# Optimization experiments

Measured on AMD Instinct MI355X. Metric: run time of the kernel, lower is better.

The kernel has to match this reference:

```python
import jax, jax.numpy as jnp
import numpy as np

B, S, E, H, W, G = 1, 2048, 1024, 16, 512, 16
HD = E // H

def setup_inputs() -> dict:
    key = jax.random.key(0)
    ks = jax.random.split(key, 12)
    s = 1.0 / np.sqrt(E)
    inp = {
        'query': jax.random.normal(ks[0], (B, S, E), jnp.float32),
        'key':   jax.random.normal(ks[1], (B, S, E), jnp.float32),
        'value': jax.random.normal(ks[2], (B, S, E), jnp.float32),
        'is_global': jnp.broadcast_to(jnp.arange(S) < G, (B, S)),
        'Wq': jax.random.uniform(ks[3], (E, E), jnp.float32, -s, s),
        'bq': jax.random.uniform(ks[4], (E,),   jnp.float32, -s, s),
        'Wk': jax.random.uniform(ks[5], (E, E), jnp.float32, -s, s),
        'bk': jax.random.uniform(ks[6], (E,),   jnp.float32, -s, s),
        'Wv': jax.random.uniform(ks[7], (E, E), jnp.float32, -s, s),
        'bv': jax.random.uniform(ks[8], (E,),   jnp.float32, -s, s),
        'Wo': jax.random.uniform(ks[9], (E, E), jnp.float32, -s, s),
        'bo': jax.random.uniform(ks[10], (E,),  jnp.float32, -s, s),
    }
    return inp

def reference(query, key, value, is_global, Wq, bq, Wk, bk, Wv, bv, Wo, bo):
    # Linear projections (torch Linear: x @ W.T + b), reshape to [B,H,S,HD]
    def proj(x, Wt, b):
        return (x @ Wt.T + b).reshape(B, S, H, HD).transpose(0, 2, 1, 3)
    q = proj(query, Wq, bq)
    k = proj(key,   Wk, bk)
    v = proj(value, Wv, bv)

    scores = jnp.einsum('bhqd,bhkd->bhqk', q, k) / np.sqrt(HD)  # [B,H,S,S]

    idx = jnp.arange(S)
    window_mask = jnp.abs(idx[None, :] - idx[:, None]) <= W      # [S,S]
    combined = (window_mask[None, None]
                | is_global[:, None, None, :]    # global keys
                | is_global[:, None, :, None])   # global queries
    scores = jnp.where(combined, scores, -jnp.inf)

    attn = jax.nn.softmax(scores, axis=-1)  # dropout is identity in eval
    out = jnp.einsum('bhqk,bhkd->bhqd', attn, v)
    out = out.transpose(0, 2, 1, 3).reshape(B, S, E)
    return out @ Wo.T + bo
```

## Files before the change

kernel.cpp:

```cpp
#include <hip/hip_runtime.h>
#include <hip/hip_bf16.h>
#include <stdint.h>

#define S_LEN 2048
#define E_DIM 1024
#define N_HEAD 16
#define HD 64
#define WIN 512

typedef __attribute__((ext_vector_type(4))) float f32x4;
typedef __attribute__((ext_vector_type(8))) short bf16x8;
typedef __attribute__((ext_vector_type(8))) unsigned short u16x8;

__device__ __forceinline__ unsigned f2bf2(float lo, float hi) {
  __hip_bfloat162 h = __float22bfloat162_rn(make_float2(lo, hi));
  return *reinterpret_cast<unsigned*>(&h);
}
__device__ __forceinline__ unsigned short f2bf(float f) {
  __hip_bfloat16 h = __float2bfloat16(f);
  return *reinterpret_cast<unsigned short*>(&h);
}
__device__ __forceinline__ float bf2f(unsigned short u) {
  union { unsigned u; float f; } v; v.u = (unsigned)u << 16; return v.f;
}

__device__ __forceinline__ void gl2lds16(const void* g, void* l) {
  __builtin_amdgcn_global_load_lds((const __attribute__((address_space(1))) void*)g,
                                   (__attribute__((address_space(3))) void*)l, 16, 0, 0);
}

__global__ __launch_bounds__(256) void convert_kernel(
    const float* __restrict__ q, const float* __restrict__ k, const float* __restrict__ v,
    const float* __restrict__ wq, const float* __restrict__ wk,
    const float* __restrict__ wv, const float* __restrict__ wo,
    unsigned short* __restrict__ dst, const int* __restrict__ gm,
    unsigned char* __restrict__ kmask, unsigned char* __restrict__ bflag) {
  const size_t SE = (size_t)S_LEN * E_DIM, EE = (size_t)E_DIM * E_DIM;
  if (blockIdx.x == 0) {
    __shared__ int badw;
    int tid = threadIdx.x;
    if (tid == 0) badw = 0;
    __syncthreads();
    for (int i = tid; i < S_LEN / 4; i += 256) {
      int vv = gm[i];
      if (vv != 0 && vv != 1) atomicOr(&badw, 1);
    }
    __syncthreads();
    const int bytes = badw;
    const unsigned char* gb = (const unsigned char*)gm;
    for (int i = tid; i < S_LEN; i += 256)
      kmask[i] = bytes ? (unsigned char)(gb[i] != 0) : (unsigned char)(gm[i] != 0);
    if (tid < S_LEN / 64) {
      unsigned char any = 0;
      for (int j = 0; j < 64; ++j) {
        int i = tid * 64 + j;
        any |= bytes ? (unsigned char)(gb[i] != 0) : (unsigned char)(gm[i] != 0);
      }
      bflag[tid] = any;
    }
  }
  size_t i = ((size_t)blockIdx.x * 256 + threadIdx.x) * 8;
  const float* src;
  size_t off;
  if (i < SE) { src = q; off = i; }
  else if (i < 2 * SE) { src = k; off = i - SE; }
  else if (i < 3 * SE) { src = v; off = i - 2 * SE; }
  else if (i < 3 * SE + EE) { src = wq; off = i - 3 * SE; }
  else if (i < 3 * SE + 2 * EE) { src = wk; off = i - 3 * SE - EE; }
  else if (i < 3 * SE + 3 * EE) { src = wv; off = i - 3 * SE - 2 * EE; }
  else { src = wo; off = i - 3 * SE - 3 * EE; }
  f32x4 x0 = *(const f32x4*)(src + off);
  f32x4 x1 = *(const f32x4*)(src + off + 4);
  union { u16x8 v; unsigned u[4]; } o;
  o.u[0] = f2bf2(x0[0], x0[1]); o.u[1] = f2bf2(x0[2], x0[3]);
  o.u[2] = f2bf2(x1[0], x1[1]); o.u[3] = f2bf2(x1[2], x1[3]);
  *(u16x8*)(dst + i) = o.v;
}

template <int BN, int OUTMODE>
__device__ __forceinline__ void gemm_body(const unsigned short* __restrict__ A,
                                          const unsigned short* __restrict__ B,
                                          const float* __restrict__ bias,
                                          void* __restrict__ Out_) {
  __shared__ unsigned short As[64][64];
  __shared__ unsigned short Bs[BN][64];
  constexpr int MI = (BN == 128) ? 2 : 1;
  const int tid = threadIdx.x;
  const int wid = tid >> 6, lane = tid & 63;
  const int a = lane & 15, g = lane >> 4;
  const int m0 = blockIdx.y * 64, n0 = blockIdx.x * BN;
  const int wr = (BN == 128) ? (wid >> 1) * 32 : wid * 16;
  const int wc = (BN == 128) ? (wid & 1) * 64 : 0;
  const int l8 = lane >> 3, l7 = (lane & 7) * 8;
  f32x4 acc[MI][4] = {};

  for (int k0 = 0; k0 < E_DIM; k0 += 64) {
    __syncthreads();
#pragma unroll
    for (int c = 0; c < 2; ++c) {
      const int r0 = (wid * 2 + c) * 8;
      gl2lds16(A + (size_t)(m0 + r0 + l8) * E_DIM + k0 + l7, &As[r0][0]);
    }
#pragma unroll
    for (int c = 0; c < BN / 32; ++c) {
      const int r0 = (wid * (BN / 32) + c) * 8;
      gl2lds16(B + (size_t)(n0 + r0 + l8) * E_DIM + k0 + l7, &Bs[r0][0]);
    }
    __syncthreads();
#pragma unroll
    for (int s = 0; s < 2; ++s) {
      bf16x8 af[MI], bfv[4];
#pragma unroll
      for (int i = 0; i < MI; ++i) af[i] = *(const bf16x8*)&As[wr + i * 16 + a][s * 32 + g * 8];
#pragma unroll
      for (int j = 0; j < 4; ++j) bfv[j] = *(const bf16x8*)&Bs[wc + j * 16 + a][s * 32 + g * 8];
#pragma unroll
      for (int i = 0; i < MI; ++i)
#pragma unroll
        for (int j = 0; j < 4; ++j)
          acc[i][j] = __builtin_amdgcn_mfma_f32_16x16x32_bf16(af[i], bfv[j], acc[i][j], 0, 0, 0);
    }
  }
#pragma unroll
  for (int i = 0; i < MI; ++i)
#pragma unroll
    for (int j = 0; j < 4; ++j) {
      const int row0 = m0 + wr + i * 16 + g * 4;
      const int col = n0 + wc + j * 16 + a;
      if (OUTMODE == 2) {
        unsigned short* O = (unsigned short*)Out_;
        unsigned lo = f2bf2(acc[i][j][0] + bias[col], acc[i][j][1] + bias[col]);
        unsigned hi = f2bf2(acc[i][j][2] + bias[col], acc[i][j][3] + bias[col]);
        uint2 pk; pk.x = lo; pk.y = hi;
        *(uint2*)&O[(size_t)col * S_LEN + row0] = pk;
      } else {
#pragma unroll
        for (int r = 0; r < 4; ++r) {
          float v = acc[i][j][r] + bias[col];
          if (OUTMODE == 0) {
            unsigned short* O = (unsigned short*)Out_;
            O[((size_t)(col >> 6) * S_LEN + row0 + r) * HD + (col & 63)] = f2bf(v);
          } else {
            float* O = (float*)Out_;
            O[(size_t)(row0 + r) * E_DIM + col] = v;
          }
        }
      }
    }
}

__global__ __launch_bounds__(256) void gemm_qkv_kernel(
    const unsigned short* __restrict__ wsbf, const float* __restrict__ bq,
    const float* __restrict__ bk, const float* __restrict__ bv,
    unsigned short* __restrict__ Qo, unsigned short* __restrict__ Ko,
    unsigned short* __restrict__ Vo) {
  const size_t SE = (size_t)S_LEN * E_DIM, EE = (size_t)E_DIM * E_DIM;
  const int z = blockIdx.z;
  const unsigned short* A = wsbf + (size_t)z * SE;
  const unsigned short* W = wsbf + 3 * SE + (size_t)z * EE;
  const float* b = z == 0 ? bq : (z == 1 ? bk : bv);
  if (z == 2)
    gemm_body<128, 2>(A, W, b, Vo);
  else
    gemm_body<128, 0>(A, W, b, z == 0 ? Qo : Ko);
}

__global__ __launch_bounds__(256) void gemm_out_kernel(
    const unsigned short* __restrict__ Oi, const unsigned short* __restrict__ Wo,
    const float* __restrict__ bo, float* __restrict__ out) {
  gemm_body<64, 1>(Oi, Wo, bo, out);
}

__global__ __launch_bounds__(256) void attn_kernel(
    const unsigned short* __restrict__ Q, const unsigned short* __restrict__ K,
    const unsigned short* __restrict__ Vt_g, const unsigned char* __restrict__ kmask,
    const unsigned char* __restrict__ bflag, unsigned short* __restrict__ O,
    unsigned short* __restrict__ PA, float2* __restrict__ ML) {
  __shared__ unsigned short Kt[128][72];
  __shared__ unsigned short Vt[64][136];
  __shared__ float Plf[4][16][132];
  __shared__ unsigned char kmAll[S_LEN];

  const int tid = threadIdx.x;
  const int wid = tid >> 6, lane = tid & 63;
  const int a = lane & 15, g = lane >> 4;

  if (blockIdx.x >= 32) {
    const int h = blockIdx.y;
    const int split = (blockIdx.x - 32) * 4 + wid;
    const int k0 = split * 64;
    const unsigned short* Kh = K + (size_t)h * S_LEN * HD;
    const unsigned short* Vh = Vt_g + (size_t)h * HD * S_LEN;
    const float c = 0.18033688011112042f;

    const size_t qb = ((size_t)h * S_LEN + a) * HD;
    const bf16x8 qf0 = *(const bf16x8*)(Q + qb + g * 8);
    const bf16x8 qf1 = *(const bf16x8*)(Q + qb + 32 + g * 8);

    f32x4 s4[4];
#pragma unroll
    for (int t = 0; t < 4; ++t) {
      const unsigned short* kp = Kh + (size_t)(k0 + t * 16 + a) * HD;
      bf16x8 kf0 = *(const bf16x8*)(kp + g * 8);
      bf16x8 kf1 = *(const bf16x8*)(kp + 32 + g * 8);
      f32x4 z = {0.f, 0.f, 0.f, 0.f};
      z = __builtin_amdgcn_mfma_f32_16x16x32_bf16(qf0, kf0, z, 0, 0, 0);
      z = __builtin_amdgcn_mfma_f32_16x16x32_bf16(qf1, kf1, z, 0, 0, 0);
      s4[t] = z;
    }
    float m[4], l[4], tv[4][4];
#pragma unroll
    for (int t = 0; t < 4; ++t)
#pragma unroll
      for (int r = 0; r < 4; ++r) tv[t][r] = s4[t][r] * c;
#pragma unroll
    for (int r = 0; r < 4; ++r) {
      float tm = fmaxf(fmaxf(tv[0][r], tv[1][r]), fmaxf(tv[2][r], tv[3][r]));
#pragma unroll
      for (int off = 1; off < 16; off <<= 1) tm = fmaxf(tm, __shfl_xor(tm, off, 16));
      float ps = 0.f;
#pragma unroll
      for (int t = 0; t < 4; ++t) {
        float p = __builtin_amdgcn_exp2f(tv[t][r] - tm);
        tv[t][r] = p; ps += p;
      }
#pragma unroll
      for (int off = 1; off < 16; off <<= 1) ps += __shfl_xor(ps, off, 16);
      m[r] = tm; l[r] = ps;
    }
#pragma unroll
    for (int t = 0; t < 4; ++t)
#pragma unroll
      for (int r = 0; r < 4; ++r)
        Plf[wid][g * 4 + r][t * 16 + a] = tv[t][r];
    bf16x8 pa[2];
#pragma unroll
    for (int ks = 0; ks < 2; ++ks) {
      const float* pp = &Plf[wid][a][ks * 32 + g * 8];
      f32x4 x0 = *(const f32x4*)pp, x1 = *(const f32x4*)(pp + 4);
      union { bf16x8 v; unsigned u[4]; } pu;
      pu.u[0] = f2bf2(x0[0], x0[1]); pu.u[1] = f2bf2(x0[2], x0[3]);
      pu.u[2] = f2bf2(x1[0], x1[1]); pu.u[3] = f2bf2(x1[2], x1[3]);
      pa[ks] = pu.v;
    }
    f32x4 acc[4] = {};
#pragma unroll
    for (int d = 0; d < 4; ++d)
#pragma unroll
      for (int ks = 0; ks < 2; ++ks) {
        bf16x8 vf = *(const bf16x8*)(Vh + (size_t)(d * 16 + a) * S_LEN + k0 + ks * 32 + g * 8);
        acc[d] = __builtin_amdgcn_mfma_f32_16x16x32_bf16(pa[ks], vf, acc[d], 0, 0, 0);
      }
    unsigned short* pacc = PA + (((size_t)h * 32 + split) * 16) * 64;
#pragma unroll
    for (int d = 0; d < 4; ++d)
#pragma unroll
      for (int r = 0; r < 4; ++r)
        pacc[(g * 4 + r) * 64 + d * 16 + a] = f2bf(acc[d][r]);
    if (a == 0) {
      float2* pml = ML + ((size_t)h * 32 + split) * 16;
#pragma unroll
      for (int r = 0; r < 4; ++r) pml[g * 4 + r] = make_float2(m[r], l[r]);
    }
    return;
  }

  const int fid = blockIdx.x + (blockIdx.y << 5);
  const int logical = ((fid & 7) << 6) + (fid >> 3);
  const int h = logical >> 5;
  const int q0 = (logical & 31) << 6;
  const int qw = q0 + wid * 16;

  ((uint2*)kmAll)[tid] = ((const uint2*)kmask)[tid];

  const size_t qbase = ((size_t)h * S_LEN + (qw + a)) * HD;
  const bf16x8 qf0 = *(const bf16x8*)(Q + qbase + g * 8);
  const bf16x8 qf1 = *(const bf16x8*)(Q + qbase + 32 + g * 8);

  __syncthreads();
  int qg[4];
#pragma unroll
  for (int r = 0; r < 4; ++r) qg[r] = kmAll[qw + g * 4 + r];

  unsigned amask = 0;
  {
    int lo = (q0 - WIN) >> 7; if (lo < 0) lo = 0;
    int hi = (q0 + 63 + WIN) >> 7; if (hi > 15) hi = 15;
#pragma unroll
    for (int t2 = 0; t2 < 16; ++t2) {
      bool act = (t2 >= lo && t2 <= hi) || bflag[2 * t2] || bflag[2 * t2 + 1];
      amask |= (unsigned)act << t2;
    }
  }

  float m[4], l[4];
  f32x4 acc[4];
#pragma unroll
  for (int r = 0; r < 4; ++r) { m[r] = -1e30f; l[r] = 0.f; }
#pragma unroll
  for (int d = 0; d < 4; ++d) acc[d] = f32x4{0.f, 0.f, 0.f, 0.f};

  const unsigned short* Kh = K + (size_t)h * S_LEN * HD;
  const unsigned short* Vh = Vt_g + (size_t)h * HD * S_LEN;
  const float c = 0.18033688011112042f;

  u16x8 kreg[4], vreg[4];
  auto issue = [&](int k0) {
    const u16x8* pk = (const u16x8*)(Kh + (size_t)(k0 + (tid >> 1)) * HD + (tid & 1) * 32);
    kreg[0] = pk[0]; kreg[1] = pk[1]; kreg[2] = pk[2]; kreg[3] = pk[3];
    const u16x8* pv = (const u16x8*)(Vh + (size_t)(tid >> 2) * S_LEN + k0 + (tid & 3) * 32);
    vreg[0] = pv[0]; vreg[1] = pv[1]; vreg[2] = pv[2]; vreg[3] = pv[3];
  };

  int kb = amask ? __builtin_ctz(amask) : 16;
  if (kb < 16) issue(kb * 128);
  while (kb < 16) {
    const unsigned rem = amask >> (kb + 1);
    const int nxt = rem ? kb + 1 + __builtin_ctz(rem) : 16;
    const int k0 = kb * 128;

    __syncthreads();
    {
      u16x8* dk = (u16x8*)&Kt[tid >> 1][(tid & 1) * 32];
      dk[0] = kreg[0]; dk[1] = kreg[1]; dk[2] = kreg[2]; dk[3] = kreg[3];
      u16x8* dv = (u16x8*)&Vt[tid >> 2][(tid & 3) * 32];
      dv[0] = vreg[0]; dv[1] = vreg[1]; dv[2] = vreg[2]; dv[3] = vreg[3];
    }
    __syncthreads();
    if (nxt < 16) issue(nxt * 128);

    f32x4 s4[8];
    __builtin_amdgcn_s_setprio(1);
#pragma unroll
    for (int t = 0; t < 8; ++t) {
      bf16x8 kf0 = *(const bf16x8*)&Kt[t * 16 + a][g * 8];
      bf16x8 kf1 = *(const bf16x8*)&Kt[t * 16 + a][32 + g * 8];
      f32x4 z = {0.f, 0.f, 0.f, 0.f};
      z = __builtin_amdgcn_mfma_f32_16x16x32_bf16(qf0, kf0, z, 0, 0, 0);
      z = __builtin_amdgcn_mfma_f32_16x16x32_bf16(qf1, kf1, z, 0, 0, 0);
      s4[t] = z;
    }
    __builtin_amdgcn_s_setprio(0);

    float tv[8][4];
    const bool interior = (k0 >= q0 - 449) && (k0 <= q0 + 385);
    if (interior) {
#pragma unroll
      for (int t = 0; t < 8; ++t)
#pragma unroll
        for (int r = 0; r < 4; ++r) tv[t][r] = s4[t][r] * c;
    } else {
#pragma unroll
      for (int t = 0; t < 8; ++t) {
        const int kc = k0 + t * 16 + a;
        const int kglob = kmAll[kc];
#pragma unroll
        for (int r = 0; r < 4; ++r) {
          const int qr = qw + g * 4 + r;
          bool inc = qg[r] || kglob || ((unsigned)(qr - kc + WIN) <= (unsigned)(2 * WIN));
          tv[t][r] = inc ? s4[t][r] * c : -3.0e38f;
        }
      }
    }

    float pmax[4];
#pragma unroll
    for (int r = 0; r < 4; ++r) {
      float tm = fmaxf(fmaxf(tv[0][r], tv[1][r]), fmaxf(tv[2][r], tv[3][r]));
      tm = fmaxf(tm, fmaxf(fmaxf(tv[4][r], tv[5][r]), fmaxf(tv[6][r], tv[7][r])));
      pmax[r] = tm;
    }
    const int ok = __all((pmax[0] - m[0] <= 8.f) && (pmax[1] - m[1] <= 8.f) &&
                         (pmax[2] - m[2] <= 8.f) && (pmax[3] - m[3] <= 8.f));
    if (!ok) {
#pragma unroll
      for (int r = 0; r < 4; ++r) {
        float tm = pmax[r];
#pragma unroll
        for (int off = 1; off < 16; off <<= 1) tm = fmaxf(tm, __shfl_xor(tm, off, 16));
        const float mn = fmaxf(m[r], tm);
        const float rs = __builtin_amdgcn_exp2f(m[r] - mn);
        m[r] = mn;
        l[r] *= rs;
#pragma unroll
        for (int d = 0; d < 4; ++d) acc[d][r] *= rs;
      }
    }
#pragma unroll
    for (int r = 0; r < 4; ++r) {
      float ps = 0.f;
#pragma unroll
      for (int t = 0; t < 8; ++t) {
        float p = __builtin_amdgcn_exp2f(tv[t][r] - m[r]);
        tv[t][r] = p; ps += p;
      }
      l[r] += ps;
    }

#pragma unroll
    for (int t = 0; t < 8; ++t)
#pragma unroll
      for (int r = 0; r < 4; ++r)
        Plf[wid][g * 4 + r][t * 16 + a] = tv[t][r];
    bf16x8 pa[4];
#pragma unroll
    for (int ks = 0; ks < 4; ++ks) {
      const float* pp = &Plf[wid][a][ks * 32 + g * 8];
      f32x4 x0 = *(const f32x4*)pp, x1 = *(const f32x4*)(pp + 4);
      union { bf16x8 v; unsigned u[4]; } pu;
      pu.u[0] = f2bf2(x0[0], x0[1]); pu.u[1] = f2bf2(x0[2], x0[3]);
      pu.u[2] = f2bf2(x1[0], x1[1]); pu.u[3] = f2bf2(x1[2], x1[3]);
      pa[ks] = pu.v;
    }

    __builtin_amdgcn_s_setprio(1);
#pragma unroll
    for (int d = 0; d < 4; ++d)
#pragma unroll
      for (int ks = 0; ks < 4; ++ks) {
        bf16x8 vf = *(const bf16x8*)&Vt[d * 16 + a][ks * 32 + g * 8];
        acc[d] = __builtin_amdgcn_mfma_f32_16x16x32_bf16(pa[ks], vf, acc[d], 0, 0, 0);
      }
    __builtin_amdgcn_s_setprio(0);
    kb = nxt;
  }

#pragma unroll
  for (int r = 0; r < 4; ++r) {
#pragma unroll
    for (int off = 1; off < 16; off <<= 1) l[r] += __shfl_xor(l[r], off, 16);
  }
#pragma unroll
  for (int d = 0; d < 4; ++d)
#pragma unroll
    for (int r = 0; r < 4; ++r) {
      const int qr = qw + g * 4 + r;
      float v = acc[d][r] / l[r];
      O[(size_t)qr * E_DIM + h * HD + d * 16 + a] = f2bf(v);
    }
}

__global__ __launch_bounds__(256) void combine_glb_kernel(
    const unsigned short* __restrict__ PA, const float2* __restrict__ ML,
    unsigned short* __restrict__ O) {
  const int h = blockIdx.x, tid = threadIdx.x;
  const int row = tid >> 4, d0 = (tid & 15) * 4;
  float M = -1e30f;
#pragma unroll 8
  for (int s = 0; s < 32; ++s) M = fmaxf(M, ML[((size_t)h * 32 + s) * 16 + row].x);
  float L = 0.f, o0 = 0.f, o1 = 0.f, o2 = 0.f, o3 = 0.f;
  for (int s = 0; s < 32; ++s) {
    float2 ml = ML[((size_t)h * 32 + s) * 16 + row];
    float w = __builtin_amdgcn_exp2f(ml.x - M);
    L += w * ml.y;
    const unsigned short* p = PA + (((size_t)h * 32 + s) * 16 + row) * 64 + d0;
    o0 += w * bf2f(p[0]); o1 += w * bf2f(p[1]);
    o2 += w * bf2f(p[2]); o3 += w * bf2f(p[3]);
  }
  const float inv = 1.0f / L;
  uint2 pk;
  pk.x = f2bf2(o0 * inv, o1 * inv);
  pk.y = f2bf2(o2 * inv, o3 * inv);
  *(uint2*)&O[(size_t)row * E_DIM + h * HD + d0] = pk;
}

extern "C" void kernel_launch(void* const* d_in, const int* in_sizes, int n_in,
                              void* d_out, int out_size, void* d_ws, size_t ws_size,
                              hipStream_t stream) {
  const float* q  = (const float*)d_in[0];
  const float* k  = (const float*)d_in[1];
  const float* v  = (const float*)d_in[2];
  const int* isg  = (const int*)d_in[3];
  const float* Wq = (const float*)d_in[4];
  const float* bq = (const float*)d_in[5];
  const float* Wk = (const float*)d_in[6];
  const float* bk = (const float*)d_in[7];
  const float* Wv = (const float*)d_in[8];
  const float* bv = (const float*)d_in[9];
  const float* Wo = (const float*)d_in[10];
  const float* bo = (const float*)d_in[11];

  const size_t SE = (size_t)S_LEN * E_DIM, EE = (size_t)E_DIM * E_DIM;
  unsigned short* wsbf = (unsigned short*)d_ws;
  unsigned short* Qb = wsbf + 3 * SE + 4 * EE;
  unsigned short* Kb = Qb + SE;
  unsigned short* Vb = Kb + SE;
  unsigned short* Ob = wsbf;
  unsigned char* kmask = (unsigned char*)(Vb + SE);
  unsigned char* bflag = kmask + S_LEN;
  unsigned short* PA = wsbf + SE;
  float2* ML = (float2*)(PA + (size_t)16 * 32 * 16 * 64);

  const int total_conv_blocks = (int)((3 * SE + 4 * EE) / (256 * 8));
  convert_kernel<<<total_conv_blocks, 256, 0, stream>>>(q, k, v, Wq, Wk, Wv, Wo, wsbf,
                                                        isg, kmask, bflag);
  gemm_qkv_kernel<<<dim3(E_DIM / 128, S_LEN / 64, 3), 256, 0, stream>>>(
      wsbf, bq, bk, bv, Qb, Kb, Vb);
  attn_kernel<<<dim3(40, N_HEAD), 256, 0, stream>>>(Qb, Kb, Vb, kmask, bflag, Ob, PA, ML);
  combine_glb_kernel<<<N_HEAD, 256, 0, stream>>>(PA, ML, Ob);
  gemm_out_kernel<<<dim3(E_DIM / 64, S_LEN / 64), 256, 0, stream>>>(
      Ob, wsbf + 3 * SE + 3 * EE, bo, (float*)d_out);
}
```

Measured before the change: 111.3 us.

## Fuse fp32-to-bf16 conversion into GEMM tile loads and drop convert kernel

Removes the standalone conversion kernel. The QKV and output GEMMs now read fp32 activations and weights directly and convert them to bf16 while staging tiles into padded LDS. The global-mask preprocessing moves into one block of the QKV GEMM. This avoids writing and re-reading a full bf16 copy of all inputs and saves one launch. In exchange, the GEMMs fetch fp32 data repeatedly across tiles and lose the async global-to-LDS loads.

```diff
diff --git a/kernel.cpp b/kernel.cpp
--- a/kernel.cpp
+++ b/kernel.cpp
@@ -29,61 +29,28 @@
                                    (__attribute__((address_space(3))) void*)l, 16, 0, 0);
 }
 
-__global__ __launch_bounds__(256) void convert_kernel(
-    const float* __restrict__ q, const float* __restrict__ k, const float* __restrict__ v,
-    const float* __restrict__ wq, const float* __restrict__ wk,
-    const float* __restrict__ wv, const float* __restrict__ wo,
-    unsigned short* __restrict__ dst, const int* __restrict__ gm,
-    unsigned char* __restrict__ kmask, unsigned char* __restrict__ bflag) {
-  const size_t SE = (size_t)S_LEN * E_DIM, EE = (size_t)E_DIM * E_DIM;
-  if (blockIdx.x == 0) {
-    __shared__ int badw;
-    int tid = threadIdx.x;
-    if (tid == 0) badw = 0;
-    __syncthreads();
-    for (int i = tid; i < S_LEN / 4; i += 256) {
-      int vv = gm[i];
-      if (vv != 0 && vv != 1) atomicOr(&badw, 1);
-    }
-    __syncthreads();
-    const int bytes = badw;
-    const unsigned char* gb = (const unsigned char*)gm;
-    for (int i = tid; i < S_LEN; i += 256)
-      kmask[i] = bytes ? (unsigned char)(gb[i] != 0) : (unsigned char)(gm[i] != 0);
-    if (tid < S_LEN / 64) {
-      unsigned char any = 0;
-      for (int j = 0; j < 64; ++j) {
-        int i = tid * 64 + j;
-        any |= bytes ? (unsigned char)(gb[i] != 0) : (unsigned char)(gm[i] != 0);
-      }
-      bflag[tid] = any;
-    }
-  }
-  size_t i = ((size_t)blockIdx.x * 256 + threadIdx.x) * 8;
-  const float* src;
-  size_t off;
-  if (i < SE) { src = q; off = i; }
-  else if (i < 2 * SE) { src = k; off = i - SE; }
-  else if (i < 3 * SE) { src = v; off = i - 2 * SE; }
-  else if (i < 3 * SE + EE) { src = wq; off = i - 3 * SE; }
-  else if (i < 3 * SE + 2 * EE) { src = wk; off = i - 3 * SE - EE; }
-  else if (i < 3 * SE + 3 * EE) { src = wv; off = i - 3 * SE - 2 * EE; }
-  else { src = wo; off = i - 3 * SE - 3 * EE; }
-  f32x4 x0 = *(const f32x4*)(src + off);
-  f32x4 x1 = *(const f32x4*)(src + off + 4);
-  union { u16x8 v; unsigned u[4]; } o;
-  o.u[0] = f2bf2(x0[0], x0[1]); o.u[1] = f2bf2(x0[2], x0[3]);
-  o.u[2] = f2bf2(x1[0], x1[1]); o.u[3] = f2bf2(x1[2], x1[3]);
-  *(u16x8*)(dst + i) = o.v;
-}
-
-template <int BN, int OUTMODE>
-__device__ __forceinline__ void gemm_body(const unsigned short* __restrict__ A,
-                                          const unsigned short* __restrict__ B,
+__device__ __forceinline__ void cvt16(const float* src, unsigned short* d0,
+                                      unsigned short* d1) {
+  f32x4 x0 = *(const f32x4*)src, x1 = *(const f32x4*)(src + 4);
+  f32x4 x2 = *(const f32x4*)(src + 8), x3 = *(const f32x4*)(src + 12);
+  union { u16x8 v; unsigned u[4]; } a, b;
+  a.u[0] = f2bf2(x0[0], x0[1]); a.u[1] = f2bf2(x0[2], x0[3]);
+  a.u[2] = f2bf2(x1[0], x1[1]); a.u[3] = f2bf2(x1[2], x1[3]);
+  b.u[0] = f2bf2(x2[0], x2[1]); b.u[1] = f2bf2(x2[2], x2[3]);
+  b.u[2] = f2bf2(x3[0], x3[1]); b.u[3] = f2bf2(x3[2], x3[3]);
+  *(u16x8*)d0 = a.v;
+  *(u16x8*)d1 = b.v;
+}
+
+template <int BN, int OUTMODE, bool AF32, bool BF32>
+__device__ __forceinline__ void gemm_body(const void* __restrict__ A_,
+                                          const void* __restrict__ B_,
                                           const float* __restrict__ bias,
                                           void* __restrict__ Out_) {
-  __shared__ unsigned short As[64][64];
-  __shared__ unsigned short Bs[BN][64];
+  constexpr int AP = AF32 ? 72 : 64;
+  constexpr int BP = BF32 ? 72 : 64;
+  __shared__ unsigned short As[64][AP];
+  __shared__ unsigned short Bs[BN][BP];
   constexpr int MI = (BN == 128) ? 2 : 1;
   const int tid = threadIdx.x;
   const int wid = tid >> 6, lane = tid & 63;
@@ -92,19 +59,39 @@
   const int wr = (BN == 128) ? (wid >> 1) * 32 : wid * 16;
   const int wc = (BN == 128) ? (wid & 1) * 64 : 0;
   const int l8 = lane >> 3, l7 = (lane & 7) * 8;
+  const int arow = tid >> 2, acol = (tid & 3) * 16;
   f32x4 acc[MI][4] = {};
 
   for (int k0 = 0; k0 < E_DIM; k0 += 64) {
     __syncthreads();
-#pragma unroll
-    for (int c = 0; c < 2; ++c) {
-      const int r0 = (wid * 2 + c) * 8;
-      gl2lds16(A + (size_t)(m0 + r0 + l8) * E_DIM + k0 + l7, &As[r0][0]);
-    }
-#pragma unroll
-    for (int c = 0; c < BN / 32; ++c) {
-      const int r0 = (wid * (BN / 32) + c) * 8;
-      gl2lds16(B + (size_t)(n0 + r0 + l8) * E_DIM + k0 + l7, &Bs[r0][0]);
+    if (AF32) {
+      const float* A = (const float*)A_;
+      cvt16(A + (size_t)(m0 + arow) * E_DIM + k0 + acol, &As[arow][acol], &As[arow][acol + 8]);
+    } else {
+      const unsigned short* A = (const unsigned short*)A_;
+#pragma unroll
+      for (int c = 0; c < 2; ++c) {
+        const int r0 = (wid * 2 + c) * 8;
+        gl2lds16(A + (size_t)(m0 + r0 + l8) * E_DIM + k0 + l7, &As[r0][0]);
+      }
+    }
+    if (BF32) {
+      const float* B = (const float*)B_;
+      if (BN == 128) {
+        const int brow = tid >> 1, bcol = (tid & 1) * 32;
+        cvt16(B + (size_t)(n0 + brow) * E_DIM + k0 + bcol, &Bs[brow][bcol], &Bs[brow][bcol + 8]);
+        cvt16(B + (size_t)(n0 + brow) * E_DIM + k0 + bcol + 16, &Bs[brow][bcol + 16],
+              &Bs[brow][bcol + 24]);
+      } else {
+        cvt16(B + (size_t)(n0 + arow) * E_DIM + k0 + acol, &Bs[arow][acol], &Bs[arow][acol + 8]);
+      }
+    } else {
+      const unsigned short* B = (const unsigned short*)B_;
+#pragma unroll
+      for (int c = 0; c < BN / 32; ++c) {
+        const int r0 = (wid * (BN / 32) + c) * 8;
+        gl2lds16(B + (size_t)(n0 + r0 + l8) * E_DIM + k0 + l7, &Bs[r0][0]);
+      }
     }
     __syncthreads();
 #pragma unroll
@@ -150,25 +137,50 @@
 }
 
 __global__ __launch_bounds__(256) void gemm_qkv_kernel(
-    const unsigned short* __restrict__ wsbf, const float* __restrict__ bq,
-    const float* __restrict__ bk, const float* __restrict__ bv,
+    const float* __restrict__ q, const float* __restrict__ k, const float* __restrict__ v,
+    const float* __restrict__ Wq, const float* __restrict__ Wk, const float* __restrict__ Wv,
+    const float* __restrict__ bq, const float* __restrict__ bk, const float* __restrict__ bv,
     unsigned short* __restrict__ Qo, unsigned short* __restrict__ Ko,
-    unsigned short* __restrict__ Vo) {
-  const size_t SE = (size_t)S_LEN * E_DIM, EE = (size_t)E_DIM * E_DIM;
+    unsigned short* __restrict__ Vo, const int* __restrict__ gm,
+    unsigned char* __restrict__ kmask, unsigned char* __restrict__ bflag) {
   const int z = blockIdx.z;
-  const unsigned short* A = wsbf + (size_t)z * SE;
-  const unsigned short* W = wsbf + 3 * SE + (size_t)z * EE;
+  if (z == 0 && blockIdx.x == 0 && blockIdx.y == 0) {
+    __shared__ int badw;
+    int tid = threadIdx.x;
+    if (tid == 0) badw = 0;
+    __syncthreads();
+    for (int i = tid; i < S_LEN / 4; i += 256) {
+      int vv = gm[i];
+      if (vv != 0 && vv != 1) atomicOr(&badw, 1);
+    }
+    __syncthreads();
+    const int bytes = badw;
+    const unsigned char* gb = (const unsigned char*)gm;
+    for (int i = tid; i < S_LEN; i += 256)
+      kmask[i] = bytes ? (unsigned char)(gb[i] != 0) : (unsigned char)(gm[i] != 0);
+    if (tid < S_LEN / 64) {
+      unsigned char any = 0;
+      for (int j = 0; j < 64; ++j) {
+        int i = tid * 64 + j;
+        any |= bytes ? (unsigned char)(gb[i] != 0) : (unsigned char)(gm[i] != 0);
+      }
+      bflag[tid] = any;
+    }
+    __syncthreads();
+  }
+  const float* A = z == 0 ? q : (z == 1 ? k : v);
+  const float* W = z == 0 ? Wq : (z == 1 ? Wk : Wv);
   const float* b = z == 0 ? bq : (z == 1 ? bk : bv);
   if (z == 2)
-    gemm_body<128, 2>(A, W, b, Vo);
+    gemm_body<128, 2, true, true>(A, W, b, Vo);
   else
-    gemm_body<128, 0>(A, W, b, z == 0 ? Qo : Ko);
+    gemm_body<128, 0, true, true>(A, W, b, z == 0 ? Qo : Ko);
 }
 
 __global__ __launch_bounds__(256) void gemm_out_kernel(
-    const unsigned short* __restrict__ Oi, const unsigned short* __restrict__ Wo,
+    const unsigned short* __restrict__ Oi, const float* __restrict__ Wo,
     const float* __restrict__ bo, float* __restrict__ out) {
-  gemm_body<64, 1>(Oi, Wo, bo, out);
+  gemm_body<64, 1, false, true>(Oi, Wo, bo, out);
 }
 
 __global__ __launch_bounds__(256) void attn_kernel(
@@ -491,13 +503,10 @@
   unsigned short* PA = wsbf + SE;
   float2* ML = (float2*)(PA + (size_t)16 * 32 * 16 * 64);
 
-  const int total_conv_blocks = (int)((3 * SE + 4 * EE) / (256 * 8));
-  convert_kernel<<<total_conv_blocks, 256, 0, stream>>>(q, k, v, Wq, Wk, Wv, Wo, wsbf,
-                                                        isg, kmask, bflag);
   gemm_qkv_kernel<<<dim3(E_DIM / 128, S_LEN / 64, 3), 256, 0, stream>>>(
-      wsbf, bq, bk, bv, Qb, Kb, Vb);
+      q, k, v, Wq, Wk, Wv, bq, bk, bv, Qb, Kb, Vb, isg, kmask, bflag);
   attn_kernel<<<dim3(40, N_HEAD), 256, 0, stream>>>(Qb, Kb, Vb, kmask, bflag, Ob, PA, ML);
   combine_glb_kernel<<<N_HEAD, 256, 0, stream>>>(PA, ML, Ob);
   gemm_out_kernel<<<dim3(E_DIM / 64, S_LEN / 64), 256, 0, stream>>>(
-      Ob, wsbf + 3 * SE + 3 * EE, bo, (float*)d_out);
-}
+      Ob, Wo, bo, (float*)d_out);
+}
```

Measured after the change: 145.0 us. +30.2%, slower.

## Fuse global-query split-K combine into attention kernel with per-wave online softmax

Applied to the files above, without the earlier changes.

Global-query rows are now handled by one block per head, where each wave runs an online softmax over 512 keys and the four waves merge through shared memory. Before, 8 blocks per head wrote bf16 partials and (m,l) pairs to global memory for a separate combine kernel. This removes a kernel launch and the global round-trip of partials. The cost is less parallelism: each head's global rows now run serially through 8 chunks in a single block, which may become the tail of the grid. Local blocks also skip writing global rows to avoid a race.

```diff
diff --git a/kernel.cpp b/kernel.cpp
--- a/kernel.cpp
+++ b/kernel.cpp
@@ -174,8 +174,7 @@
 __global__ __launch_bounds__(256) void attn_kernel(
     const unsigned short* __restrict__ Q, const unsigned short* __restrict__ K,
     const unsigned short* __restrict__ Vt_g, const unsigned char* __restrict__ kmask,
-    const unsigned char* __restrict__ bflag, unsigned short* __restrict__ O,
-    unsigned short* __restrict__ PA, float2* __restrict__ ML) {
+    const unsigned char* __restrict__ bflag, unsigned short* __restrict__ O) {
   __shared__ unsigned short Kt[128][72];
   __shared__ unsigned short Vt[64][136];
   __shared__ float Plf[4][16][132];
@@ -185,10 +184,8 @@
   const int wid = tid >> 6, lane = tid & 63;
   const int a = lane & 15, g = lane >> 4;
 
-  if (blockIdx.x >= 32) {
+  if (blockIdx.x == 32) {
     const int h = blockIdx.y;
-    const int split = (blockIdx.x - 32) * 4 + wid;
-    const int k0 = split * 64;
     const unsigned short* Kh = K + (size_t)h * S_LEN * HD;
     const unsigned short* Vh = Vt_g + (size_t)h * HD * S_LEN;
     const float c = 0.18033688011112042f;
@@ -197,70 +194,109 @@
     const bf16x8 qf0 = *(const bf16x8*)(Q + qb + g * 8);
     const bf16x8 qf1 = *(const bf16x8*)(Q + qb + 32 + g * 8);
 
-    f32x4 s4[4];
-#pragma unroll
-    for (int t = 0; t < 4; ++t) {
-      const unsigned short* kp = Kh + (size_t)(k0 + t * 16 + a) * HD;
-      bf16x8 kf0 = *(const bf16x8*)(kp + g * 8);
-      bf16x8 kf1 = *(const bf16x8*)(kp + 32 + g * 8);
-      f32x4 z = {0.f, 0.f, 0.f, 0.f};
-      z = __builtin_amdgcn_mfma_f32_16x16x32_bf16(qf0, kf0, z, 0, 0, 0);
-      z = __builtin_amdgcn_mfma_f32_16x16x32_bf16(qf1, kf1, z, 0, 0, 0);
-      s4[t] = z;
-    }
-    float m[4], l[4], tv[4][4];
-#pragma unroll
-    for (int t = 0; t < 4; ++t)
-#pragma unroll
-      for (int r = 0; r < 4; ++r) tv[t][r] = s4[t][r] * c;
-#pragma unroll
-    for (int r = 0; r < 4; ++r) {
-      float tm = fmaxf(fmaxf(tv[0][r], tv[1][r]), fmaxf(tv[2][r], tv[3][r]));
-#pragma unroll
-      for (int off = 1; off < 16; off <<= 1) tm = fmaxf(tm, __shfl_xor(tm, off, 16));
-      float ps = 0.f;
+    float m[4], l[4];
+    f32x4 acc[4];
+#pragma unroll
+    for (int r = 0; r < 4; ++r) { m[r] = -1e30f; l[r] = 0.f; }
+#pragma unroll
+    for (int d = 0; d < 4; ++d) acc[d] = f32x4{0.f, 0.f, 0.f, 0.f};
+
+    for (int ch = 0; ch < 8; ++ch) {
+      const int k0 = wid * 512 + ch * 64;
+      f32x4 s4[4];
 #pragma unroll
       for (int t = 0; t < 4; ++t) {
-        float p = __builtin_amdgcn_exp2f(tv[t][r] - tm);
-        tv[t][r] = p; ps += p;
-      }
-#pragma unroll
-      for (int off = 1; off < 16; off <<= 1) ps += __shfl_xor(ps, off, 16);
-      m[r] = tm; l[r] = ps;
-    }
-#pragma unroll
-    for (int t = 0; t < 4; ++t)
+        const unsigned short* kp = Kh + (size_t)(k0 + t * 16 + a) * HD;
+        bf16x8 kf0 = *(const bf16x8*)(kp + g * 8);
+        bf16x8 kf1 = *(const bf16x8*)(kp + 32 + g * 8);
+        f32x4 z = {0.f, 0.f, 0.f, 0.f};
+        z = __builtin_amdgcn_mfma_f32_16x16x32_bf16(qf0, kf0, z, 0, 0, 0);
+        z = __builtin_amdgcn_mfma_f32_16x16x32_bf16(qf1, kf1, z, 0, 0, 0);
+        s4[t] = z;
+      }
+      float tv[4][4];
+#pragma unroll
+      for (int t = 0; t < 4; ++t)
+#pragma unroll
+        for (int r = 0; r < 4; ++r) tv[t][r] = s4[t][r] * c;
+#pragma unroll
+      for (int r = 0; r < 4; ++r) {
+        float tm = fmaxf(fmaxf(tv[0][r], tv[1][r]), fmaxf(tv[2][r], tv[3][r]));
+#pragma unroll
+        for (int off = 1; off < 16; off <<= 1) tm = fmaxf(tm, __shfl_xor(tm, off, 16));
+        const float mn = fmaxf(m[r], tm);
+        const float rs = __builtin_amdgcn_exp2f(m[r] - mn);
+        m[r] = mn;
+        float ps = 0.f;
+#pragma unroll
+        for (int t = 0; t < 4; ++t) {
+          float p = __builtin_amdgcn_exp2f(tv[t][r] - mn);
+          tv[t][r] = p; ps += p;
+        }
+#pragma unroll
+        for (int off = 1; off < 16; off <<= 1) ps += __shfl_xor(ps, off, 16);
+        l[r] = l[r] * rs + ps;
+#pragma unroll
+        for (int d = 0; d < 4; ++d) acc[d][r] *= rs;
+      }
+#pragma unroll
+      for (int t = 0; t < 4; ++t)
+#pragma unroll
+        for (int r = 0; r < 4; ++r)
+          Plf[wid][g * 4 + r][t * 16 + a] = tv[t][r];
+      bf16x8 pa[2];
+#pragma unroll
+      for (int ks = 0; ks < 2; ++ks) {
+        const float* pp = &Plf[wid][a][ks * 32 + g * 8];
+        f32x4 x0 = *(const f32x4*)pp, x1 = *(const f32x4*)(pp + 4);
+        union { bf16x8 v; unsigned u[4]; } pu;
+        pu.u[0] = f2bf2(x0[0], x0[1]); pu.u[1] = f2bf2(x0[2], x0[3]);
+        pu.u[2] = f2bf2(x1[0], x1[1]); pu.u[3] = f2bf2(x1[2], x1[3]);
+        pa[ks] = pu.v;
+      }
+#pragma unroll
+      for (int d = 0; d < 4; ++d)
+#pragma unroll
+        for (int ks = 0; ks < 2; ++ks) {
+          bf16x8 vf = *(const bf16x8*)(Vh + (size_t)(d * 16 + a) * S_LEN + k0 + ks * 32 + g * 8);
+          acc[d] = __builtin_amdgcn_mfma_f32_16x16x32_bf16(pa[ks], vf, acc[d], 0, 0, 0);
+        }
+    }
+
+#pragma unroll
+    for (int d = 0; d < 4; ++d)
 #pragma unroll
       for (int r = 0; r < 4; ++r)
-        Plf[wid][g * 4 + r][t * 16 + a] = tv[t][r];
-    bf16x8 pa[2];
-#pragma unroll
-    for (int ks = 0; ks < 2; ++ks) {
-      const float* pp = &Plf[wid][a][ks * 32 + g * 8];
-      f32x4 x0 = *(const f32x4*)pp, x1 = *(const f32x4*)(pp + 4);
-      union { bf16x8 v; unsigned u[4]; } pu;
-      pu.u[0] = f2bf2(x0[0], x0[1]); pu.u[1] = f2bf2(x0[2], x0[3]);
-      pu.u[2] = f2bf2(x1[0], x1[1]); pu.u[3] = f2bf2(x1[2], x1[3]);
-      pa[ks] = pu.v;
-    }
-    f32x4 acc[4] = {};
-#pragma unroll
-    for (int d = 0; d < 4; ++d)
-#pragma unroll
-      for (int ks = 0; ks < 2; ++ks) {
-        bf16x8 vf = *(const bf16x8*)(Vh + (size_t)(d * 16 + a) * S_LEN + k0 + ks * 32 + g * 8);
-        acc[d] = __builtin_amdgcn_mfma_f32_16x16x32_bf16(pa[ks], vf, acc[d], 0, 0, 0);
-      }
-    unsigned short* pacc = PA + (((size_t)h * 32 + split) * 16) * 64;
-#pragma unroll
-    for (int d = 0; d < 4; ++d)
-#pragma unroll
-      for (int r = 0; r < 4; ++r)
-        pacc[(g * 4 + r) * 64 + d * 16 + a] = f2bf(acc[d][r]);
+        Plf[wid][g * 4 + r][64 + d * 16 + a] = acc[d][r];
     if (a == 0) {
-      float2* pml = ML + ((size_t)h * 32 + split) * 16;
-#pragma unroll
-      for (int r = 0; r < 4; ++r) pml[g * 4 + r] = make_float2(m[r], l[r]);
+#pragma unroll
+      for (int r = 0; r < 4; ++r) {
+        Plf[wid][g * 4 + r][128] = m[r];
+        Plf[wid][g * 4 + r][129] = l[r];
+      }
+    }
+    __syncthreads();
+
+    {
+      const int row = tid >> 4, d0q = (tid & 15) * 4;
+      float M = Plf[0][row][128];
+#pragma unroll
+      for (int w = 1; w < 4; ++w) M = fmaxf(M, Plf[w][row][128]);
+      float L = 0.f, o0 = 0.f, o1 = 0.f, o2 = 0.f, o3 = 0.f;
+#pragma unroll
+      for (int w = 0; w < 4; ++w) {
+        const float wg = __builtin_amdgcn_exp2f(Plf[w][row][128] - M);
+        L += wg * Plf[w][row][129];
+        o0 += wg * Plf[w][row][64 + d0q];
+        o1 += wg * Plf[w][row][64 + d0q + 1];
+        o2 += wg * Plf[w][row][64 + d0q + 2];
+        o3 += wg * Plf[w][row][64 + d0q + 3];
+      }
+      const float inv = 1.0f / L;
+      uint2 pk;
+      pk.x = f2bf2(o0 * inv, o1 * inv);
+      pk.y = f2bf2(o2 * inv, o3 * inv);
+      *(uint2*)&O[(size_t)row * E_DIM + h * HD + d0q] = pk;
     }
     return;
   }
@@ -434,34 +470,11 @@
   for (int d = 0; d < 4; ++d)
 #pragma unroll
     for (int r = 0; r < 4; ++r) {
+      if (qg[r]) continue;
       const int qr = qw + g * 4 + r;
       float v = acc[d][r] / l[r];
       O[(size_t)qr * E_DIM + h * HD + d * 16 + a] = f2bf(v);
     }
-}
-
-__global__ __launch_bounds__(256) void combine_glb_kernel(
-    const unsigned short* __restrict__ PA, const float2* __restrict__ ML,
-    unsigned short* __restrict__ O) {
-  const int h = blockIdx.x, tid = threadIdx.x;
-  const int row = tid >> 4, d0 = (tid & 15) * 4;
-  float M = -1e30f;
-#pragma unroll 8
-  for (int s = 0; s < 32; ++s) M = fmaxf(M, ML[((size_t)h * 32 + s) * 16 + row].x);
-  float L = 0.f, o0 = 0.f, o1 = 0.f, o2 = 0.f, o3 = 0.f;
-  for (int s = 0; s < 32; ++s) {
-    float2 ml = ML[((size_t)h * 32 + s) * 16 + row];
-    float w = __builtin_amdgcn_exp2f(ml.x - M);
-    L += w * ml.y;
-    const unsigned short* p = PA + (((size_t)h * 32 + s) * 16 + row) * 64 + d0;
-    o0 += w * bf2f(p[0]); o1 += w * bf2f(p[1]);
-    o2 += w * bf2f(p[2]); o3 += w * bf2f(p[3]);
-  }
-  const float inv = 1.0f / L;
-  uint2 pk;
-  pk.x = f2bf2(o0 * inv, o1 * inv);
-  pk.y = f2bf2(o2 * inv, o3 * inv);
-  *(uint2*)&O[(size_t)row * E_DIM + h * HD + d0] = pk;
 }
 
 extern "C" void kernel_launch(void* const* d_in, const int* in_sizes, int n_in,
@@ -488,16 +501,13 @@
   unsigned short* Ob = wsbf;
   unsigned char* kmask = (unsigned char*)(Vb + SE);
   unsigned char* bflag = kmask + S_LEN;
-  unsigned short* PA = wsbf + SE;
-  float2* ML = (float2*)(PA + (size_t)16 * 32 * 16 * 64);
 
   const int total_conv_blocks = (int)((3 * SE + 4 * EE) / (256 * 8));
   convert_kernel<<<total_conv_blocks, 256, 0, stream>>>(q, k, v, Wq, Wk, Wv, Wo, wsbf,
                                                         isg, kmask, bflag);
   gemm_qkv_kernel<<<dim3(E_DIM / 128, S_LEN / 64, 3), 256, 0, stream>>>(
       wsbf, bq, bk, bv, Qb, Kb, Vb);
-  attn_kernel<<<dim3(40, N_HEAD), 256, 0, stream>>>(Qb, Kb, Vb, kmask, bflag, Ob, PA, ML);
-  combine_glb_kernel<<<N_HEAD, 256, 0, stream>>>(PA, ML, Ob);
+  attn_kernel<<<dim3(33, N_HEAD), 256, 0, stream>>>(Qb, Kb, Vb, kmask, bflag, Ob);
   gemm_out_kernel<<<dim3(E_DIM / 64, S_LEN / 64), 256, 0, stream>>>(
       Ob, wsbf + 3 * SE + 3 * EE, bo, (float*)d_out);
 }
```

Result: faster. 101.6 us (-8.8%).
